# Kernel optimization log

Measured on AMD Instinct MI355X. Metric: run time of the kernel, lower is better.

## Reference

```python
import jax, jax.numpy as jnp
import numpy as np

H = 16
D_MODEL = 1024
D_K = D_MODEL // H


def setup_inputs() -> dict:
    key = jax.random.key(0)
    ks = jax.random.split(key, 12)
    B, S = 4, 2048
    scale = 1.0 / np.sqrt(D_MODEL)
    inp = {
        "query": jax.random.normal(ks[0], (B, S, D_MODEL), dtype=jnp.float32),
        "key": jax.random.normal(ks[1], (B, S, D_MODEL), dtype=jnp.float32),
        "value": jax.random.normal(ks[2], (B, S, D_MODEL), dtype=jnp.float32),
        "Wq": jax.random.normal(ks[3], (D_MODEL, D_MODEL), dtype=jnp.float32) * scale,
        "bq": jnp.zeros((D_MODEL,), dtype=jnp.float32),
        "Wk": jax.random.normal(ks[4], (D_MODEL, D_MODEL), dtype=jnp.float32) * scale,
        "bk": jnp.zeros((D_MODEL,), dtype=jnp.float32),
        "Wv": jax.random.normal(ks[5], (D_MODEL, D_MODEL), dtype=jnp.float32) * scale,
        "bv": jnp.zeros((D_MODEL,), dtype=jnp.float32),
        "Wo": jax.random.normal(ks[6], (D_MODEL, D_MODEL), dtype=jnp.float32) * scale,
        "bo": jnp.zeros((D_MODEL,), dtype=jnp.float32),
    }
    return inp


def reference(query, key, value, Wq, bq, Wk, bk, Wv, bv, Wo, bo):
    B, S, _ = query.shape
    # Linear projections (torch Linear: x @ W^T + b), then split heads -> [B,H,S,d_k]
    def proj(x, W, b):
        y = x @ W.T + b
        return y.reshape(B, S, H, D_K).transpose(0, 2, 1, 3)

    q = proj(query, Wq, bq)
    k = proj(key, Wk, bk)
    v = proj(value, Wv, bv)

    # Explicit QK^T / sqrt(d_k), softmax, AV (no mask; dropout = identity in eval)
    scores = jnp.einsum("bhqd,bhkd->bhqk", q, k) / jnp.sqrt(jnp.float32(D_K))
    attn = jax.nn.softmax(scores, axis=-1)
    x = jnp.einsum("bhqk,bhkd->bhqd", attn, v)

    # Merge heads and final output projection
    x = x.transpose(0, 2, 1, 3).reshape(B, S, H * D_K)
    return x @ Wo.T + bo
```

## Files before the change

kernel.cpp:

```cpp
#include <hip/hip_runtime.h>
#include <hip/hip_bf16.h>
#include <stdint.h>

#define BATCH 4
#define SEQ   2048
#define DM    1024
#define NH    16
#define DK    64
#define MROWS (BATCH * SEQ)

#define C1 0.1803368801111204f

typedef __attribute__((ext_vector_type(8))) short short8;
typedef __attribute__((ext_vector_type(4))) float f32x4;
typedef __attribute__((ext_vector_type(4))) float floatv4;
typedef __attribute__((ext_vector_type(4))) unsigned short us4;
typedef __attribute__((ext_vector_type(4))) unsigned int uint4v;

static __device__ __forceinline__ unsigned short f2bf(float f) {
    union { float f; uint32_t u; } c; c.f = f;
    uint32_t u = c.u;
    return (unsigned short)((u + 0x7fffu + ((u >> 16) & 1u)) >> 16);
}

static __device__ __forceinline__ unsigned int cvt_pk_bf16(float a, float b) {
    __hip_bfloat162 h = __float22bfloat162_rn(float2{a, b});
    unsigned int u; __builtin_memcpy(&u, &h, 4); return u;
}

static __device__ __forceinline__ float ex2(float x) { return __builtin_amdgcn_exp2f(x); }

#define AS1C(p) ((const __attribute__((address_space(1))) unsigned int*)(uintptr_t)(const void*)(p))
#define AS3(p)  ((__attribute__((address_space(3))) unsigned int*)(uintptr_t)(void*)(p))

__global__ __launch_bounds__(256) void cvt3_k(const float* __restrict__ a, const float* __restrict__ b,
                                              const float* __restrict__ c,
                                              unsigned short* __restrict__ oa, unsigned short* __restrict__ ob,
                                              unsigned short* __restrict__ oc) {
    const int z = blockIdx.y;
    const float* s = (z == 0) ? a : (z == 1) ? b : c;
    unsigned short* o = (z == 0) ? oa : (z == 1) ? ob : oc;
    int i = blockIdx.x * 256 + threadIdx.x;
    floatv4 v = ((const floatv4*)s)[i];
    us4 w; w.x = f2bf(v.x); w.y = f2bf(v.y); w.z = f2bf(v.z); w.w = f2bf(v.w);
    ((us4*)o)[i] = w;
}

__global__ __launch_bounds__(256) void cvt4_k(const float* __restrict__ a, const float* __restrict__ b,
                                              const float* __restrict__ c, const float* __restrict__ d,
                                              unsigned short* __restrict__ oa, unsigned short* __restrict__ ob,
                                              unsigned short* __restrict__ oc, unsigned short* __restrict__ od) {
    const int z = blockIdx.y;
    const float* s = (z == 0) ? a : (z == 1) ? b : (z == 2) ? c : d;
    unsigned short* o = (z == 0) ? oa : (z == 1) ? ob : (z == 2) ? oc : od;
    int i = blockIdx.x * 256 + threadIdx.x;
    floatv4 v = ((const floatv4*)s)[i];
    us4 w; w.x = f2bf(v.x); w.y = f2bf(v.y); w.z = f2bf(v.z); w.w = f2bf(v.w);
    ((us4*)o)[i] = w;
}

static __device__ __forceinline__ void gemm_body(const unsigned short* __restrict__ A,
                                                 const unsigned short* __restrict__ Bw,
                                                 const float* __restrict__ bias,
                                                 void* __restrict__ out, int m0, int n0,
                                                 float scale, int mode) {
    constexpr int K = DM;
    constexpr int NK = K / 32;

    const int tid = threadIdx.x;
    const int wave = tid >> 6, lane = tid & 63, quad = lane >> 4, l16 = lane & 15;
    const int wm = wave >> 1, wn = wave & 1;

    __shared__ alignas(16) unsigned short As[3][256 * 32];
    __shared__ alignas(16) unsigned short Bs[3][128 * 32];

    f32x4 acc[4][4];
    #pragma unroll
    for (int i = 0; i < 4; i++)
        #pragma unroll
        for (int j = 0; j < 4; j++) acc[i][j] = (f32x4){0.f, 0.f, 0.f, 0.f};

    const int scol8 = (((lane & 3) ^ ((lane >> 3) & 3))) * 8;
    const unsigned short* Ag0 = A  + (size_t)(m0 + wave * 32 + (lane >> 2)) * K + scol8;
    const unsigned short* Ag1 = Ag0 + (size_t)16 * K;
    const unsigned short* Bg0 = Bw + (size_t)(n0 + wave * 16 + (lane >> 2)) * K + scol8;

    const int rsw = (quad ^ ((l16 >> 1) & 3)) * 8;

    short8 af[4], bfr[4];

#define GX_STG(b, kt)                                                                     \
    {   unsigned short* as_ = &As[b][0];                                                  \
        unsigned short* bs_ = &Bs[b][0];                                                  \
        __builtin_amdgcn_global_load_lds(AS1C(Ag0 + (size_t)(kt) * 32),                   \
                                         AS3(as_ + (wave * 32) * 32), 16, 0, 0);          \
        __builtin_amdgcn_global_load_lds(AS1C(Ag1 + (size_t)(kt) * 32),                   \
                                         AS3(as_ + (wave * 32 + 16) * 32), 16, 0, 0);     \
        __builtin_amdgcn_global_load_lds(AS1C(Bg0 + (size_t)(kt) * 32),                   \
                                         AS3(bs_ + (wave * 16) * 32), 16, 0, 0); }

#define GX_LD(b)                                                                          \
    {   const unsigned short* ar_ = &As[b][0];                                            \
        const unsigned short* br_ = &Bs[b][0];                                            \
        _Pragma("unroll")                                                                 \
        for (int i_ = 0; i_ < 4; i_++) af[i_]  = *(const short8*)&ar_[(wm * 64 + i_ * 16 + l16) * 32 + rsw]; \
        _Pragma("unroll")                                                                 \
        for (int j_ = 0; j_ < 4; j_++) bfr[j_] = *(const short8*)&br_[(wn * 64 + j_ * 16 + l16) * 32 + rsw]; }

#define GX_MMA                                                                            \
    {   __builtin_amdgcn_s_setprio(1);                                                    \
        _Pragma("unroll")                                                                 \
        for (int i_ = 0; i_ < 4; i_++)                                                    \
            _Pragma("unroll")                                                             \
            for (int j_ = 0; j_ < 4; j_++)                                                \
                acc[i_][j_] = __builtin_amdgcn_mfma_f32_16x16x32_bf16(af[i_], bfr[j_], acc[i_][j_], 0, 0, 0); \
        __builtin_amdgcn_s_setprio(0); }

#define GX_VM3  { asm volatile("s_waitcnt vmcnt(3)" ::: "memory"); }
#define GX_VM0  { asm volatile("s_waitcnt vmcnt(0)" ::: "memory"); }
#define GX_BAR  __builtin_amdgcn_s_barrier()
#define GX_SB0  __builtin_amdgcn_sched_barrier(0)
#define GX_LG0  { asm volatile("s_waitcnt lgkmcnt(0)" ::: "memory"); __builtin_amdgcn_sched_barrier(0); }

    GX_STG(0, 0);
    GX_STG(1, 1);
    int bc = 0;
    #pragma unroll 1
    for (int k = 0; k < NK - 1; ++k) {
        GX_VM3; GX_BAR; GX_SB0;
        if (k + 2 < NK) {
            int bp = bc + 2; if (bp >= 3) bp -= 3;
            GX_STG(bp, k + 2);
        }
        GX_LD(bc); GX_LG0; GX_MMA;
        bc = (bc == 2) ? 0 : bc + 1;
    }
    GX_VM0; GX_BAR; GX_SB0;
    GX_LD(bc); GX_LG0; GX_MMA;

#undef GX_STG
#undef GX_LD
#undef GX_MMA
#undef GX_VM3
#undef GX_VM0
#undef GX_BAR
#undef GX_SB0
#undef GX_LG0

    #pragma unroll
    for (int nf = 0; nf < 4; nf++) {
        const int n = n0 + wn * 64 + nf * 16 + l16;
        const float bv = bias[n];
        if (mode == 2) {
            const int bb = m0 >> 11;
            const int hh = n >> 6, dd = n & (DK - 1);
            unsigned short* obase = (unsigned short*)out
                                  + (((size_t)bb * NH + hh) * DK + dd) * SEQ
                                  + (m0 & (SEQ - 1)) + wm * 64 + quad * 8;
            #pragma unroll
            for (int mf = 0; mf < 4; mf++) {
                us4 w;
                #pragma unroll
                for (int r = 0; r < 4; r++) w[r] = f2bf(acc[mf][nf][r] + bv);
                *(us4*)(obase + (mf >> 1) * 32 + (mf & 1) * 4) = w;
            }
        } else {
            const int hh = n >> 6, dd = n & (DK - 1);
            #pragma unroll
            for (int mf = 0; mf < 4; mf++) {
                #pragma unroll
                for (int r = 0; r < 4; r++) {
                    const int mrow = m0 + wm * 64 + mf * 16 + quad * 4 + r;
                    float val = (acc[mf][nf][r] + bv) * scale;
                    if (mode == 0) {
                        int bb = mrow >> 11, ss = mrow & (SEQ - 1);
                        ((unsigned short*)out)[((((size_t)bb * NH + hh) * SEQ + ss) << 6) + dd] = f2bf(val);
                    } else {
                        ((float*)out)[(size_t)mrow * DM + n] = val;
                    }
                }
            }
        }
    }
}

__global__ __launch_bounds__(512, 4) void gemm_qkv_k(const unsigned short* qa, const unsigned short* ka,
                                                     const unsigned short* va, const unsigned short* wq,
                                                     const unsigned short* wk, const unsigned short* wv,
                                                     const float* bq, const float* bk, const float* bv,
                                                     unsigned short* qh, unsigned short* kh,
                                                     unsigned short* vtc) {
    const int z = blockIdx.z;
    const unsigned short* A = (z == 0) ? qa : (z == 1) ? ka : va;
    const unsigned short* W = (z == 0) ? wq : (z == 1) ? wk : wv;
    const float* bi = (z == 0) ? bq : (z == 1) ? bk : bv;
    void* o = (z == 0) ? (void*)qh : (z == 1) ? (void*)kh : (void*)vtc;
    const float sc = (z == 0) ? C1 : 1.0f;
    const int mode = (z == 2) ? 2 : 0;
    gemm_body(A, W, bi, o, blockIdx.x * 256, blockIdx.y * 128, sc, mode);
}

__global__ __launch_bounds__(512, 4) void gemm_o_k(const unsigned short* xb, const unsigned short* wo,
                                                   const float* bo, float* out) {
    gemm_body(xb, wo, bo, out, blockIdx.x * 256, blockIdx.y * 128, 1.0f, 1);
}

__global__ __launch_bounds__(256, 2) void flash_attn_k(const unsigned short* __restrict__ Qh,
                                                       const unsigned short* __restrict__ Kh,
                                                       const unsigned short* __restrict__ Vtc,
                                                       unsigned short* __restrict__ Xb) {
    const int tid = threadIdx.x;
    const int wave = tid >> 6, lane = tid & 63, quad = lane >> 4, l16 = lane & 15;
    const int h = blockIdx.y, b = blockIdx.z;
    const unsigned short* Qp = Qh  + (size_t)(b * NH + h) * SEQ * DK;
    const unsigned short* Kp = Kh  + (size_t)(b * NH + h) * SEQ * DK;
    const unsigned short* Vp = Vtc + (size_t)(b * NH + h) * DK * SEQ;
    const int q0 = blockIdx.x * 256 + wave * 64;

    __shared__ alignas(16) unsigned short kt[2][128][72];
    __shared__ alignas(16) unsigned short vt[2][64][136];

    short8 aq[4][2];
    #pragma unroll
    for (int m = 0; m < 4; m++)
        #pragma unroll
        for (int kk = 0; kk < 2; kk++)
            aq[m][kk] = *(const short8*)(Qp + (size_t)(q0 + m * 16 + l16) * DK + kk * 32 + quad * 8);

    short8 ones;
    #pragma unroll
    for (int j = 0; j < 8; j++) ones[j] = (short)0x3F80;

    f32x4 O[4][4];
    f32x4 lacc[4];
    #pragma unroll
    for (int m = 0; m < 4; m++) {
        #pragma unroll
        for (int db = 0; db < 4; db++) O[m][db] = (f32x4){0.f, 0.f, 0.f, 0.f};
        lacc[m] = (f32x4){0.f, 0.f, 0.f, 0.f};
    }

    const unsigned short* kgp = Kp + (size_t)(tid >> 3) * DK + (tid & 7) * 8;
    const unsigned short* vgp = Vp + (size_t)(tid >> 4) * SEQ + (tid & 15) * 8;
    unsigned short* kws0 = &kt[0][tid >> 3][(tid & 7) * 8];
    unsigned short* vws0 = &vt[0][tid >> 4][(tid & 15) * 8];

    short8 krg[4], vrg[4];
    #pragma unroll
    for (int it = 0; it < 4; it++) {
        krg[it] = *(const short8*)(kgp + (size_t)it * 32 * DK);
        vrg[it] = *(const short8*)(vgp + (size_t)it * 16 * SEQ);
    }
    kgp += (size_t)128 * DK;
    vgp += 128;
    #pragma unroll
    for (int it = 0; it < 4; it++) {
        *(short8*)(kws0 + it * 32 * 72) = krg[it];
        *(short8*)(vws0 + it * 16 * 136) = vrg[it];
    }
    #pragma unroll
    for (int it = 0; it < 4; it++) {
        krg[it] = *(const short8*)(kgp + (size_t)it * 32 * DK);
        vrg[it] = *(const short8*)(vgp + (size_t)it * 16 * SEQ);
    }
    kgp += (size_t)128 * DK;
    vgp += 128;
    asm volatile("s_waitcnt lgkmcnt(0)" ::: "memory");
    __builtin_amdgcn_s_barrier();
    __builtin_amdgcn_sched_barrier(0);

#define FLASH_TILE(cur)                                                                   \
    {   _Pragma("unroll")                                                                 \
        for (int it = 0; it < 4; it++) {                                                  \
            *(short8*)(kws0 + ((cur) ^ 1) * 128 * 72 + it * 32 * 72) = krg[it];           \
            *(short8*)(vws0 + ((cur) ^ 1) * 64 * 136 + it * 16 * 136) = vrg[it];          \
        }                                                                                 \
        _Pragma("unroll")                                                                 \
        for (int it = 0; it < 4; it++) {                                                  \
            krg[it] = *(const short8*)(kgp + (size_t)it * 32 * DK);                       \
            vrg[it] = *(const short8*)(vgp + (size_t)it * 16 * SEQ);                      \
        }                                                                                 \
        kgp += (size_t)128 * DK;                                                          \
        vgp += 128;                                                                       \
        _Pragma("unroll")                                                                 \
        for (int t = 0; t < 4; t++) {                                                     \
            f32x4 s[4][2];                                                                \
            _Pragma("unroll")                                                             \
            for (int m = 0; m < 4; m++) {                                                 \
                s[m][0] = (f32x4){0.f, 0.f, 0.f, 0.f};                                    \
                s[m][1] = (f32x4){0.f, 0.f, 0.f, 0.f};                                    \
            }                                                                             \
            _Pragma("unroll")                                                             \
            for (int kk = 0; kk < 2; kk++) {                                              \
                short8 bk0 = *(const short8*)&kt[cur][(t * 2    ) * 16 + l16][kk * 32 + quad * 8]; \
                short8 bk1 = *(const short8*)&kt[cur][(t * 2 + 1) * 16 + l16][kk * 32 + quad * 8]; \
                _Pragma("unroll")                                                         \
                for (int m = 0; m < 4; m++) {                                             \
                    s[m][0] = __builtin_amdgcn_mfma_f32_16x16x32_bf16(bk0, aq[m][kk], s[m][0], 0, 0, 0); \
                    s[m][1] = __builtin_amdgcn_mfma_f32_16x16x32_bf16(bk1, aq[m][kk], s[m][1], 0, 0, 0); \
                }                                                                         \
            }                                                                             \
            short8 pa[4];                                                                 \
            _Pragma("unroll")                                                             \
            for (int m = 0; m < 4; m++) {                                                 \
                uint4v pk;                                                                \
                pk.x = cvt_pk_bf16(ex2(s[m][0][0]), ex2(s[m][0][1]));                     \
                pk.y = cvt_pk_bf16(ex2(s[m][0][2]), ex2(s[m][0][3]));                     \
                pk.z = cvt_pk_bf16(ex2(s[m][1][0]), ex2(s[m][1][1]));                     \
                pk.w = cvt_pk_bf16(ex2(s[m][1][2]), ex2(s[m][1][3]));                     \
                __builtin_memcpy(&pa[m], &pk, 16);                                        \
            }                                                                             \
            _Pragma("unroll")                                                             \
            for (int db = 0; db < 4; db++) {                                              \
                short8 vf = *(const short8*)&vt[cur][db * 16 + l16][t * 32 + quad * 8];   \
                _Pragma("unroll")                                                         \
                for (int m = 0; m < 4; m++)                                               \
                    O[m][db] = __builtin_amdgcn_mfma_f32_16x16x32_bf16(pa[m], vf, O[m][db], 0, 0, 0); \
            }                                                                             \
            _Pragma("unroll")                                                             \
            for (int m = 0; m < 4; m++)                                                   \
                lacc[m] = __builtin_amdgcn_mfma_f32_16x16x32_bf16(pa[m], ones, lacc[m], 0, 0, 0); \
        }                                                                                 \
        asm volatile("s_waitcnt lgkmcnt(0)" ::: "memory");                                \
        __builtin_amdgcn_s_barrier();                                                     \
        __builtin_amdgcn_sched_barrier(0);                                                \
    }

    #pragma unroll 1
    for (int ti = 0; ti < SEQ / 128; ti += 2) {
        FLASH_TILE(0);
        FLASH_TILE(1);
    }
#undef FLASH_TILE

    #pragma unroll
    for (int m = 0; m < 4; m++) {
        #pragma unroll
        for (int r = 0; r < 4; r++) {
            const float inv = 1.f / lacc[m][r];
            const int srow = q0 + m * 16 + quad * 4 + r;
            unsigned short* op = Xb + ((size_t)b * SEQ + srow) * DM + h * DK;
            #pragma unroll
            for (int db = 0; db < 4; db++)
                op[db * 16 + l16] = f2bf(O[m][db][r] * inv);
        }
    }
}

extern "C" void kernel_launch(void* const* d_in, const int* in_sizes, int n_in,
                              void* d_out, int out_size, void* d_ws, size_t ws_size,
                              hipStream_t stream) {
    const float* q_in = (const float*)d_in[0];
    const float* k_in = (const float*)d_in[1];
    const float* v_in = (const float*)d_in[2];
    const float* Wq   = (const float*)d_in[3];
    const float* bq   = (const float*)d_in[4];
    const float* Wk   = (const float*)d_in[5];
    const float* bk   = (const float*)d_in[6];
    const float* Wv   = (const float*)d_in[7];
    const float* bv   = (const float*)d_in[8];
    const float* Wo   = (const float*)d_in[9];
    const float* bo   = (const float*)d_in[10];

    const size_t MB = 1024ull * 1024ull;
    char* ws = (char*)d_ws;
    unsigned short* qa  = (unsigned short*)(ws +   0 * MB);
    unsigned short* ka  = (unsigned short*)(ws +  16 * MB);
    unsigned short* va  = (unsigned short*)(ws +  32 * MB);
    unsigned short* wqb = (unsigned short*)(ws +  48 * MB);
    unsigned short* wkb = (unsigned short*)(ws +  50 * MB);
    unsigned short* wvb = (unsigned short*)(ws +  52 * MB);
    unsigned short* wob = (unsigned short*)(ws +  54 * MB);
    unsigned short* qh  = (unsigned short*)(ws +  56 * MB);
    unsigned short* kh  = (unsigned short*)(ws +  72 * MB);
    unsigned short* vtc = (unsigned short*)(ws +  88 * MB);
    unsigned short* xb  = (unsigned short*)(ws + 104 * MB);

    cvt3_k<<<dim3(8192, 3), 256, 0, stream>>>(q_in, k_in, v_in, qa, ka, va);
    cvt4_k<<<dim3(1024, 4), 256, 0, stream>>>(Wq, Wk, Wv, Wo, wqb, wkb, wvb, wob);

    gemm_qkv_k<<<dim3(MROWS / 256, DM / 128, 3), 512, 0, stream>>>(qa, ka, va, wqb, wkb, wvb,
                                                                   bq, bk, bv, qh, kh, vtc);

    flash_attn_k<<<dim3(SEQ / 256, NH, BATCH), 256, 0, stream>>>(qh, kh, vtc, xb);

    gemm_o_k<<<dim3(MROWS / 256, DM / 128), 512, 0, stream>>>(xb, wob, bo, (float*)d_out);
}
```

Baseline: 331.2 us.

## Fuse fp32-to-bf16 input conversion into QKV GEMM and retile output GEMM

The separate conversion kernel for query/key/value is removed. The QKV GEMM now loads fp32 activations straight into registers, converts them to bf16 and writes them to shared memory, with A double-buffered and B staged asynchronously. This removes a full read and write pass over the activation tensors in bf16, at the cost of reading fp32 A data inside the GEMM through the register path instead of async direct-to-LDS loads. The output projection becomes its own kernel with 128x128 tiles, which doubles the block count for better occupancy and load balance.

```diff
diff --git a/kernel.cpp b/kernel.cpp
--- a/kernel.cpp
+++ b/kernel.cpp
@@ -32,19 +32,6 @@
 
 #define AS1C(p) ((const __attribute__((address_space(1))) unsigned int*)(uintptr_t)(const void*)(p))
 #define AS3(p)  ((__attribute__((address_space(3))) unsigned int*)(uintptr_t)(void*)(p))
-
-__global__ __launch_bounds__(256) void cvt3_k(const float* __restrict__ a, const float* __restrict__ b,
-                                              const float* __restrict__ c,
-                                              unsigned short* __restrict__ oa, unsigned short* __restrict__ ob,
-                                              unsigned short* __restrict__ oc) {
-    const int z = blockIdx.y;
-    const float* s = (z == 0) ? a : (z == 1) ? b : c;
-    unsigned short* o = (z == 0) ? oa : (z == 1) ? ob : oc;
-    int i = blockIdx.x * 256 + threadIdx.x;
-    floatv4 v = ((const floatv4*)s)[i];
-    us4 w; w.x = f2bf(v.x); w.y = f2bf(v.y); w.z = f2bf(v.z); w.w = f2bf(v.w);
-    ((us4*)o)[i] = w;
-}
 
 __global__ __launch_bounds__(256) void cvt4_k(const float* __restrict__ a, const float* __restrict__ b,
                                               const float* __restrict__ c, const float* __restrict__ d,
@@ -59,11 +46,11 @@
     ((us4*)o)[i] = w;
 }
 
-static __device__ __forceinline__ void gemm_body(const unsigned short* __restrict__ A,
-                                                 const unsigned short* __restrict__ Bw,
-                                                 const float* __restrict__ bias,
-                                                 void* __restrict__ out, int m0, int n0,
-                                                 float scale, int mode) {
+static __device__ __forceinline__ void gemm_qkv_body(const float* __restrict__ A,
+                                                     const unsigned short* __restrict__ Bw,
+                                                     const float* __restrict__ bias,
+                                                     void* __restrict__ out, int m0, int n0,
+                                                     float scale, int mode) {
     constexpr int K = DM;
     constexpr int NK = K / 32;
 
@@ -71,7 +58,7 @@
     const int wave = tid >> 6, lane = tid & 63, quad = lane >> 4, l16 = lane & 15;
     const int wm = wave >> 1, wn = wave & 1;
 
-    __shared__ alignas(16) unsigned short As[3][256 * 32];
+    __shared__ alignas(16) unsigned short As[2][256 * 32];
     __shared__ alignas(16) unsigned short Bs[3][128 * 32];
 
     f32x4 acc[4][4];
@@ -81,33 +68,42 @@
         for (int j = 0; j < 4; j++) acc[i][j] = (f32x4){0.f, 0.f, 0.f, 0.f};
 
     const int scol8 = (((lane & 3) ^ ((lane >> 3) & 3))) * 8;
-    const unsigned short* Ag0 = A  + (size_t)(m0 + wave * 32 + (lane >> 2)) * K + scol8;
-    const unsigned short* Ag1 = Ag0 + (size_t)16 * K;
+    const float* Af0 = A + (size_t)(m0 + wave * 32 + (lane >> 2)) * K + scol8;
+    const float* Af1 = Af0 + (size_t)16 * K;
     const unsigned short* Bg0 = Bw + (size_t)(n0 + wave * 16 + (lane >> 2)) * K + scol8;
 
     const int rsw = (quad ^ ((l16 >> 1) & 3)) * 8;
+    const int wa0 = (wave * 32 + (lane >> 2)) * 32 + (lane & 3) * 8;
 
     short8 af[4], bfr[4];
-
-#define GX_STG(b, kt)                                                                     \
-    {   unsigned short* as_ = &As[b][0];                                                  \
-        unsigned short* bs_ = &Bs[b][0];                                                  \
-        __builtin_amdgcn_global_load_lds(AS1C(Ag0 + (size_t)(kt) * 32),                   \
-                                         AS3(as_ + (wave * 32) * 32), 16, 0, 0);          \
-        __builtin_amdgcn_global_load_lds(AS1C(Ag1 + (size_t)(kt) * 32),                   \
-                                         AS3(as_ + (wave * 32 + 16) * 32), 16, 0, 0);     \
-        __builtin_amdgcn_global_load_lds(AS1C(Bg0 + (size_t)(kt) * 32),                   \
-                                         AS3(bs_ + (wave * 16) * 32), 16, 0, 0); }
-
-#define GX_LD(b)                                                                          \
-    {   const unsigned short* ar_ = &As[b][0];                                            \
-        const unsigned short* br_ = &Bs[b][0];                                            \
-        _Pragma("unroll")                                                                 \
-        for (int i_ = 0; i_ < 4; i_++) af[i_]  = *(const short8*)&ar_[(wm * 64 + i_ * 16 + l16) * 32 + rsw]; \
-        _Pragma("unroll")                                                                 \
-        for (int j_ = 0; j_ < 4; j_++) bfr[j_] = *(const short8*)&br_[(wn * 64 + j_ * 16 + l16) * 32 + rsw]; }
-
-#define GX_MMA                                                                            \
+    floatv4 a0l, a0h, a1l, a1h;
+
+#define QV_AL(kt)                                                                         \
+    {   a0l = *(const floatv4*)(Af0 + (size_t)(kt) * 32);                                 \
+        a0h = *(const floatv4*)(Af0 + (size_t)(kt) * 32 + 4);                             \
+        a1l = *(const floatv4*)(Af1 + (size_t)(kt) * 32);                                 \
+        a1h = *(const floatv4*)(Af1 + (size_t)(kt) * 32 + 4); }
+
+#define QV_BS(b, kt)                                                                      \
+    {   __builtin_amdgcn_global_load_lds(AS1C(Bg0 + (size_t)(kt) * 32),                   \
+                                         AS3(&Bs[b][(wave * 16) * 32]), 16, 0, 0); }
+
+#define QV_AWRITE(ab)                                                                     \
+    {   uint4v p0, p1;                                                                    \
+        p0.x = cvt_pk_bf16(a0l.x, a0l.y); p0.y = cvt_pk_bf16(a0l.z, a0l.w);               \
+        p0.z = cvt_pk_bf16(a0h.x, a0h.y); p0.w = cvt_pk_bf16(a0h.z, a0h.w);               \
+        p1.x = cvt_pk_bf16(a1l.x, a1l.y); p1.y = cvt_pk_bf16(a1l.z, a1l.w);               \
+        p1.z = cvt_pk_bf16(a1h.x, a1h.y); p1.w = cvt_pk_bf16(a1h.z, a1h.w);               \
+        *(uint4v*)&As[ab][wa0] = p0;                                                      \
+        *(uint4v*)&As[ab][wa0 + 16 * 32] = p1; }
+
+#define QV_LD(ab, bb)                                                                     \
+    {   _Pragma("unroll")                                                                 \
+        for (int i_ = 0; i_ < 4; i_++) af[i_]  = *(const short8*)&As[ab][(wm * 64 + i_ * 16 + l16) * 32 + rsw]; \
+        _Pragma("unroll")                                                                 \
+        for (int j_ = 0; j_ < 4; j_++) bfr[j_] = *(const short8*)&Bs[bb][(wn * 64 + j_ * 16 + l16) * 32 + rsw]; }
+
+#define QV_MMA                                                                            \
     {   __builtin_amdgcn_s_setprio(1);                                                    \
         _Pragma("unroll")                                                                 \
         for (int i_ = 0; i_ < 4; i_++)                                                    \
@@ -116,46 +112,56 @@
                 acc[i_][j_] = __builtin_amdgcn_mfma_f32_16x16x32_bf16(af[i_], bfr[j_], acc[i_][j_], 0, 0, 0); \
         __builtin_amdgcn_s_setprio(0); }
 
-#define GX_VM3  { asm volatile("s_waitcnt vmcnt(3)" ::: "memory"); }
-#define GX_VM0  { asm volatile("s_waitcnt vmcnt(0)" ::: "memory"); }
-#define GX_BAR  __builtin_amdgcn_s_barrier()
-#define GX_SB0  __builtin_amdgcn_sched_barrier(0)
-#define GX_LG0  { asm volatile("s_waitcnt lgkmcnt(0)" ::: "memory"); __builtin_amdgcn_sched_barrier(0); }
-
-    GX_STG(0, 0);
-    GX_STG(1, 1);
-    int bc = 0;
+#define QV_SB0  __builtin_amdgcn_sched_barrier(0)
+#define QV_BAR  __builtin_amdgcn_s_barrier()
+#define QV_LG0  { asm volatile("s_waitcnt lgkmcnt(0)" ::: "memory"); __builtin_amdgcn_sched_barrier(0); }
+
+    QV_BS(0, 0); QV_SB0;
+    QV_AL(0);    QV_SB0;
+    QV_BS(1, 1); QV_SB0;
+
+    int bb = 0;
     #pragma unroll 1
     for (int k = 0; k < NK - 1; ++k) {
-        GX_VM3; GX_BAR; GX_SB0;
+        asm volatile("s_waitcnt vmcnt(1)" ::: "memory");
+        QV_SB0;
+        QV_AWRITE(k & 1);
+        QV_LG0;
+        QV_BAR; QV_SB0;
+        QV_AL(k + 1); QV_SB0;
         if (k + 2 < NK) {
-            int bp = bc + 2; if (bp >= 3) bp -= 3;
-            GX_STG(bp, k + 2);
+            int bp = bb + 2; if (bp >= 3) bp -= 3;
+            QV_BS(bp, k + 2);
         }
-        GX_LD(bc); GX_LG0; GX_MMA;
-        bc = (bc == 2) ? 0 : bc + 1;
-    }
-    GX_VM0; GX_BAR; GX_SB0;
-    GX_LD(bc); GX_LG0; GX_MMA;
-
-#undef GX_STG
-#undef GX_LD
-#undef GX_MMA
-#undef GX_VM3
-#undef GX_VM0
-#undef GX_BAR
-#undef GX_SB0
-#undef GX_LG0
+        QV_SB0;
+        QV_LD(k & 1, bb); QV_LG0; QV_MMA;
+        bb = (bb == 2) ? 0 : bb + 1;
+    }
+    asm volatile("s_waitcnt vmcnt(0)" ::: "memory");
+    QV_SB0;
+    QV_AWRITE((NK - 1) & 1);
+    QV_LG0;
+    QV_BAR; QV_SB0;
+    QV_LD((NK - 1) & 1, bb); QV_LG0; QV_MMA;
+
+#undef QV_AL
+#undef QV_BS
+#undef QV_AWRITE
+#undef QV_LD
+#undef QV_MMA
+#undef QV_SB0
+#undef QV_BAR
+#undef QV_LG0
 
     #pragma unroll
     for (int nf = 0; nf < 4; nf++) {
         const int n = n0 + wn * 64 + nf * 16 + l16;
         const float bv = bias[n];
         if (mode == 2) {
-            const int bb = m0 >> 11;
+            const int bbt = m0 >> 11;
             const int hh = n >> 6, dd = n & (DK - 1);
             unsigned short* obase = (unsigned short*)out
-                                  + (((size_t)bb * NH + hh) * DK + dd) * SEQ
+                                  + (((size_t)bbt * NH + hh) * DK + dd) * SEQ
                                   + (m0 & (SEQ - 1)) + wm * 64 + quad * 8;
             #pragma unroll
             for (int mf = 0; mf < 4; mf++) {
@@ -172,37 +178,119 @@
                 for (int r = 0; r < 4; r++) {
                     const int mrow = m0 + wm * 64 + mf * 16 + quad * 4 + r;
                     float val = (acc[mf][nf][r] + bv) * scale;
-                    if (mode == 0) {
-                        int bb = mrow >> 11, ss = mrow & (SEQ - 1);
-                        ((unsigned short*)out)[((((size_t)bb * NH + hh) * SEQ + ss) << 6) + dd] = f2bf(val);
-                    } else {
-                        ((float*)out)[(size_t)mrow * DM + n] = val;
-                    }
+                    int bbt = mrow >> 11, ss = mrow & (SEQ - 1);
+                    ((unsigned short*)out)[((((size_t)bbt * NH + hh) * SEQ + ss) << 6) + dd] = f2bf(val);
                 }
             }
         }
     }
 }
 
-__global__ __launch_bounds__(512, 4) void gemm_qkv_k(const unsigned short* qa, const unsigned short* ka,
-                                                     const unsigned short* va, const unsigned short* wq,
-                                                     const unsigned short* wk, const unsigned short* wv,
+__global__ __launch_bounds__(512, 4) void gemm_qkv_k(const float* qf, const float* kf, const float* vf,
+                                                     const unsigned short* wq, const unsigned short* wk,
+                                                     const unsigned short* wv,
                                                      const float* bq, const float* bk, const float* bv,
                                                      unsigned short* qh, unsigned short* kh,
                                                      unsigned short* vtc) {
     const int z = blockIdx.z;
-    const unsigned short* A = (z == 0) ? qa : (z == 1) ? ka : va;
+    const float* A = (z == 0) ? qf : (z == 1) ? kf : vf;
     const unsigned short* W = (z == 0) ? wq : (z == 1) ? wk : wv;
     const float* bi = (z == 0) ? bq : (z == 1) ? bk : bv;
     void* o = (z == 0) ? (void*)qh : (z == 1) ? (void*)kh : (void*)vtc;
     const float sc = (z == 0) ? C1 : 1.0f;
     const int mode = (z == 2) ? 2 : 0;
-    gemm_body(A, W, bi, o, blockIdx.x * 256, blockIdx.y * 128, sc, mode);
-}
-
-__global__ __launch_bounds__(512, 4) void gemm_o_k(const unsigned short* xb, const unsigned short* wo,
-                                                   const float* bo, float* out) {
-    gemm_body(xb, wo, bo, out, blockIdx.x * 256, blockIdx.y * 128, 1.0f, 1);
+    gemm_qkv_body(A, W, bi, o, blockIdx.x * 256, blockIdx.y * 128, sc, mode);
+}
+
+__global__ __launch_bounds__(512, 4) void gemm_o_k(const unsigned short* __restrict__ A,
+                                                   const unsigned short* __restrict__ Bw,
+                                                   const float* __restrict__ bias,
+                                                   float* __restrict__ out) {
+    constexpr int K = DM;
+    constexpr int NK = K / 32;
+    const int m0 = blockIdx.x * 128, n0 = blockIdx.y * 128;
+
+    const int tid = threadIdx.x;
+    const int wave = tid >> 6, lane = tid & 63, quad = lane >> 4, l16 = lane & 15;
+    const int wm = wave >> 2, wn = wave & 3;
+
+    __shared__ alignas(16) unsigned short As[3][128 * 32];
+    __shared__ alignas(16) unsigned short Bs[3][128 * 32];
+
+    f32x4 acc[4][2];
+    #pragma unroll
+    for (int i = 0; i < 4; i++) { acc[i][0] = (f32x4){0.f,0.f,0.f,0.f}; acc[i][1] = (f32x4){0.f,0.f,0.f,0.f}; }
+
+    const int scol8 = (((lane & 3) ^ ((lane >> 3) & 3))) * 8;
+    const unsigned short* Ag0 = A  + (size_t)(m0 + wave * 16 + (lane >> 2)) * K + scol8;
+    const unsigned short* Bg0 = Bw + (size_t)(n0 + wave * 16 + (lane >> 2)) * K + scol8;
+    const int rsw = (quad ^ ((l16 >> 1) & 3)) * 8;
+
+    short8 af[4], bfr[2];
+
+#define GO_STG(b, kt)                                                                     \
+    {   __builtin_amdgcn_global_load_lds(AS1C(Ag0 + (size_t)(kt) * 32),                   \
+                                         AS3(&As[b][(wave * 16) * 32]), 16, 0, 0);        \
+        __builtin_amdgcn_global_load_lds(AS1C(Bg0 + (size_t)(kt) * 32),                   \
+                                         AS3(&Bs[b][(wave * 16) * 32]), 16, 0, 0); }
+
+#define GO_LD(b)                                                                          \
+    {   _Pragma("unroll")                                                                 \
+        for (int i_ = 0; i_ < 4; i_++) af[i_]  = *(const short8*)&As[b][(wm * 64 + i_ * 16 + l16) * 32 + rsw]; \
+        _Pragma("unroll")                                                                 \
+        for (int j_ = 0; j_ < 2; j_++) bfr[j_] = *(const short8*)&Bs[b][(wn * 32 + j_ * 16 + l16) * 32 + rsw]; }
+
+#define GO_MMA                                                                            \
+    {   __builtin_amdgcn_s_setprio(1);                                                    \
+        _Pragma("unroll")                                                                 \
+        for (int i_ = 0; i_ < 4; i_++) {                                                  \
+            acc[i_][0] = __builtin_amdgcn_mfma_f32_16x16x32_bf16(af[i_], bfr[0], acc[i_][0], 0, 0, 0); \
+            acc[i_][1] = __builtin_amdgcn_mfma_f32_16x16x32_bf16(af[i_], bfr[1], acc[i_][1], 0, 0, 0); } \
+        __builtin_amdgcn_s_setprio(0); }
+
+#define GO_BAR  __builtin_amdgcn_s_barrier()
+#define GO_SB0  __builtin_amdgcn_sched_barrier(0)
+#define GO_LG0  { asm volatile("s_waitcnt lgkmcnt(0)" ::: "memory"); __builtin_amdgcn_sched_barrier(0); }
+
+    GO_STG(0, 0);
+    GO_STG(1, 1);
+    int bc = 0;
+    #pragma unroll 1
+    for (int k = 0; k < NK - 1; ++k) {
+        asm volatile("s_waitcnt vmcnt(2)" ::: "memory");
+        GO_BAR; GO_SB0;
+        if (k + 2 < NK) {
+            int bp = bc + 2; if (bp >= 3) bp -= 3;
+            GO_STG(bp, k + 2);
+        }
+        GO_SB0;
+        GO_LD(bc); GO_LG0; GO_MMA;
+        bc = (bc == 2) ? 0 : bc + 1;
+    }
+    asm volatile("s_waitcnt vmcnt(0)" ::: "memory");
+    GO_BAR; GO_SB0;
+    GO_LD(bc); GO_LG0; GO_MMA;
+
+#undef GO_STG
+#undef GO_LD
+#undef GO_MMA
+#undef GO_BAR
+#undef GO_SB0
+#undef GO_LG0
+
+    #pragma unroll
+    for (int nf = 0; nf < 2; nf++) {
+        const int n = n0 + wn * 32 + nf * 16 + l16;
+        const float bv = bias[n];
+        #pragma unroll
+        for (int mf = 0; mf < 4; mf++) {
+            #pragma unroll
+            for (int r = 0; r < 4; r++) {
+                const int mrow = m0 + wm * 64 + mf * 16 + quad * 4 + r;
+                out[(size_t)mrow * DM + n] = acc[mf][nf][r] + bv;
+            }
+        }
+    }
 }
 
 __global__ __launch_bounds__(256, 2) void flash_attn_k(const unsigned short* __restrict__ Qh,
@@ -364,9 +452,6 @@
 
     const size_t MB = 1024ull * 1024ull;
     char* ws = (char*)d_ws;
-    unsigned short* qa  = (unsigned short*)(ws +   0 * MB);
-    unsigned short* ka  = (unsigned short*)(ws +  16 * MB);
-    unsigned short* va  = (unsigned short*)(ws +  32 * MB);
     unsigned short* wqb = (unsigned short*)(ws +  48 * MB);
     unsigned short* wkb = (unsigned short*)(ws +  50 * MB);
     unsigned short* wvb = (unsigned short*)(ws +  52 * MB);
@@ -376,13 +461,13 @@
     unsigned short* vtc = (unsigned short*)(ws +  88 * MB);
     unsigned short* xb  = (unsigned short*)(ws + 104 * MB);
 
-    cvt3_k<<<dim3(8192, 3), 256, 0, stream>>>(q_in, k_in, v_in, qa, ka, va);
     cvt4_k<<<dim3(1024, 4), 256, 0, stream>>>(Wq, Wk, Wv, Wo, wqb, wkb, wvb, wob);
 
-    gemm_qkv_k<<<dim3(MROWS / 256, DM / 128, 3), 512, 0, stream>>>(qa, ka, va, wqb, wkb, wvb,
+    gemm_qkv_k<<<dim3(MROWS / 256, DM / 128, 3), 512, 0, stream>>>(q_in, k_in, v_in,
+                                                                   wqb, wkb, wvb,
                                                                    bq, bk, bv, qh, kh, vtc);
 
     flash_attn_k<<<dim3(SEQ / 256, NH, BATCH), 256, 0, stream>>>(qh, kh, vtc, xb);
 
-    gemm_o_k<<<dim3(MROWS / 256, DM / 128), 512, 0, stream>>>(xb, wob, bo, (float*)d_out);
-}
+    gemm_o_k<<<dim3(MROWS / 128, DM / 128), 512, 0, stream>>>(xb, wob, bo, (float*)d_out);
+}
```

Result: slower. 347.1 us (+4.8%).

## Switch GEMM LDS pipeline from triple to double buffering

Applied to the files above, without the earlier changes.

The projection GEMM main loop goes from a three-stage LDS ring (prefetch two tiles ahead, wait on vmcnt(3)) to two buffers with the loop unrolled by two. Buffer indices become compile-time constants, so the modulo-3 index arithmetic disappears, and LDS use drops, which could allow more resident blocks per CU. In exchange the prefetch distance shrinks to one tile and each step waits for all outstanding global loads (vmcnt(0)), so global latency may be less well hidden.

```diff
diff --git a/kernel.cpp b/kernel.cpp
--- a/kernel.cpp
+++ b/kernel.cpp
@@ -71,8 +71,8 @@
     const int wave = tid >> 6, lane = tid & 63, quad = lane >> 4, l16 = lane & 15;
     const int wm = wave >> 1, wn = wave & 1;
 
-    __shared__ alignas(16) unsigned short As[3][256 * 32];
-    __shared__ alignas(16) unsigned short Bs[3][128 * 32];
+    __shared__ alignas(16) unsigned short As[2][256 * 32];
+    __shared__ alignas(16) unsigned short Bs[2][128 * 32];
 
     f32x4 acc[4][4];
     #pragma unroll
@@ -90,22 +90,18 @@
     short8 af[4], bfr[4];
 
 #define GX_STG(b, kt)                                                                     \
-    {   unsigned short* as_ = &As[b][0];                                                  \
-        unsigned short* bs_ = &Bs[b][0];                                                  \
-        __builtin_amdgcn_global_load_lds(AS1C(Ag0 + (size_t)(kt) * 32),                   \
-                                         AS3(as_ + (wave * 32) * 32), 16, 0, 0);          \
+    {   __builtin_amdgcn_global_load_lds(AS1C(Ag0 + (size_t)(kt) * 32),                   \
+                                         AS3(&As[b][(wave * 32) * 32]), 16, 0, 0);        \
         __builtin_amdgcn_global_load_lds(AS1C(Ag1 + (size_t)(kt) * 32),                   \
-                                         AS3(as_ + (wave * 32 + 16) * 32), 16, 0, 0);     \
+                                         AS3(&As[b][(wave * 32 + 16) * 32]), 16, 0, 0);   \
         __builtin_amdgcn_global_load_lds(AS1C(Bg0 + (size_t)(kt) * 32),                   \
-                                         AS3(bs_ + (wave * 16) * 32), 16, 0, 0); }
+                                         AS3(&Bs[b][(wave * 16) * 32]), 16, 0, 0); }
 
 #define GX_LD(b)                                                                          \
-    {   const unsigned short* ar_ = &As[b][0];                                            \
-        const unsigned short* br_ = &Bs[b][0];                                            \
+    {   _Pragma("unroll")                                                                 \
+        for (int i_ = 0; i_ < 4; i_++) af[i_]  = *(const short8*)&As[b][(wm * 64 + i_ * 16 + l16) * 32 + rsw]; \
         _Pragma("unroll")                                                                 \
-        for (int i_ = 0; i_ < 4; i_++) af[i_]  = *(const short8*)&ar_[(wm * 64 + i_ * 16 + l16) * 32 + rsw]; \
-        _Pragma("unroll")                                                                 \
-        for (int j_ = 0; j_ < 4; j_++) bfr[j_] = *(const short8*)&br_[(wn * 64 + j_ * 16 + l16) * 32 + rsw]; }
+        for (int j_ = 0; j_ < 4; j_++) bfr[j_] = *(const short8*)&Bs[b][(wn * 64 + j_ * 16 + l16) * 32 + rsw]; }
 
 #define GX_MMA                                                                            \
     {   __builtin_amdgcn_s_setprio(1);                                                    \
@@ -116,32 +112,25 @@
                 acc[i_][j_] = __builtin_amdgcn_mfma_f32_16x16x32_bf16(af[i_], bfr[j_], acc[i_][j_], 0, 0, 0); \
         __builtin_amdgcn_s_setprio(0); }
 
-#define GX_VM3  { asm volatile("s_waitcnt vmcnt(3)" ::: "memory"); }
 #define GX_VM0  { asm volatile("s_waitcnt vmcnt(0)" ::: "memory"); }
 #define GX_BAR  __builtin_amdgcn_s_barrier()
 #define GX_SB0  __builtin_amdgcn_sched_barrier(0)
 #define GX_LG0  { asm volatile("s_waitcnt lgkmcnt(0)" ::: "memory"); __builtin_amdgcn_sched_barrier(0); }
 
     GX_STG(0, 0);
-    GX_STG(1, 1);
-    int bc = 0;
     #pragma unroll 1
-    for (int k = 0; k < NK - 1; ++k) {
-        GX_VM3; GX_BAR; GX_SB0;
-        if (k + 2 < NK) {
-            int bp = bc + 2; if (bp >= 3) bp -= 3;
-            GX_STG(bp, k + 2);
-        }
-        GX_LD(bc); GX_LG0; GX_MMA;
-        bc = (bc == 2) ? 0 : bc + 1;
-    }
-    GX_VM0; GX_BAR; GX_SB0;
-    GX_LD(bc); GX_LG0; GX_MMA;
+    for (int k = 0; k < NK; k += 2) {
+        GX_VM0; GX_BAR; GX_SB0;
+        GX_STG(1, k + 1);
+        GX_LD(0); GX_LG0; GX_MMA;
+        GX_VM0; GX_BAR; GX_SB0;
+        if (k + 2 < NK) GX_STG(0, k + 2);
+        GX_LD(1); GX_LG0; GX_MMA;
+    }
 
 #undef GX_STG
 #undef GX_LD
 #undef GX_MMA
-#undef GX_VM3
 #undef GX_VM0
 #undef GX_BAR
 #undef GX_SB0
```

Measured after the change: 334.5 us. No clear change (+1.0%).
